# Performance work log

Measured on AMD Instinct MI355X. Metric: run time of the kernel, lower is better.

## Reference

```python
import jax, jax.numpy as jnp
import numpy as np


def _gcn_conv(x, src, dst, num_nodes, W, b):
    # GCNConv (PyG defaults): h = D^{-1/2} (A + I) D^{-1/2} (x @ W) + b
    h = x @ W  # [N, F_out]
    ones = jnp.ones(src.shape[0], dtype=h.dtype)
    deg = jax.ops.segment_sum(ones, dst, num_segments=num_nodes)  # in-degree incl. self loop
    dinv = jnp.where(deg > 0, jax.lax.rsqrt(deg), 0.0)
    norm = dinv[src] * dinv[dst]  # [E+N]
    msg = h[src] * norm[:, None]  # gather + scale (memory-bound)
    out = jax.ops.segment_sum(msg, dst, num_segments=num_nodes)
    return out + b


def setup_inputs() -> dict:
    key = jax.random.key(0)
    k1, k2, k3, k4 = jax.random.split(key, 4)
    N, E, D_IN, D_H, D_OUT = 100000, 1600000, 128, 64, 32
    x = jax.random.normal(k1, (N, D_IN), dtype=jnp.float32)
    edge_index = jax.random.randint(k2, (2, E), 0, N, dtype=jnp.int64)
    # Glorot-style init for weights, zero bias (as PyG reset_parameters)
    W1 = jax.random.normal(k3, (D_IN, D_H), dtype=jnp.float32) * (2.0 / (D_IN + D_H)) ** 0.5
    b1 = jnp.zeros((D_H,), dtype=jnp.float32)
    W2 = jax.random.normal(k4, (D_H, D_OUT), dtype=jnp.float32) * (2.0 / (D_H + D_OUT)) ** 0.5
    b2 = jnp.zeros((D_OUT,), dtype=jnp.float32)
    return {"x": x, "edge_index": edge_index, "W1": W1, "b1": b1, "W2": W2, "b2": b2}


def reference(x, edge_index, W1, b1, W2, b2):
    num_nodes = x.shape[0]
    # add self loops once (GCNConv default add_self_loops=True)
    loop = jnp.arange(num_nodes, dtype=edge_index.dtype)
    src = jnp.concatenate([edge_index[0], loop])
    dst = jnp.concatenate([edge_index[1], loop])
    h = jax.nn.relu(_gcn_conv(x, src, dst, num_nodes, W1, b1))
    # F.dropout(training=self.training): eval mode -> identity
    out = _gcn_conv(h, src, dst, num_nodes, W2, b2)
    return out
```

## Files before the change

### kernel.cpp

```cpp
#include <hip/hip_runtime.h>
#include <math.h>


#define THREADS 256
#define HTHREADS 512
#define PBLK 256
#define BSHIFT 8
#define AGG_NODES 64
#define CSR_LDS 2048

typedef _Float16 h8v __attribute__((ext_vector_type(8)));
typedef _Float16 h4v __attribute__((ext_vector_type(4)));

__device__ __forceinline__ int nt_ld_i(const int* p) {
    return __builtin_nontemporal_load(p);
}

__device__ __forceinline__ int detect64_block(const int* __restrict__ idx, int E,
                                              int* s_flag) {
    if (threadIdx.x == 0) *s_flag = 1;
    __syncthreads();
    int n = (E < 1024) ? E : 1024;
    for (int i = threadIdx.x; i < n; i += blockDim.x)
        if (idx[2 * i + 1] != 0) *s_flag = 0;
    __syncthreads();
    return *s_flag;
}

__global__ __launch_bounds__(HTHREADS) void k_hist(const int* __restrict__ idx, int E,
                                                   int* __restrict__ bh, int NB) {
    extern __shared__ int lh[];
    int is64 = detect64_block(idx, E, &lh[NB]);
    for (int t = threadIdx.x; t < NB; t += HTHREADS) lh[t] = 0;
    __syncthreads();
    int chunk = (E + PBLK - 1) / PBLK;
    int start = blockIdx.x * chunk;
    int end = min(start + chunk, E);
    for (int e = start + threadIdx.x; e < end; e += HTHREADS) {
        int d = is64 ? idx[2 * E + 2 * e] : idx[E + e];
        atomicAdd(&lh[d >> BSHIFT], 1);
    }
    __syncthreads();
    for (int t = threadIdx.x; t < NB; t += HTHREADS)
        bh[blockIdx.x * NB + t] = lh[t];
}

__global__ __launch_bounds__(THREADS) void k_colsum(const int* __restrict__ bh,
                                                    int* __restrict__ bcnt, int NB) {
    __shared__ int ws[4];
    int b = blockIdx.x;
    int v = bh[threadIdx.x * NB + b];
    int lane = threadIdx.x & 63, w = threadIdx.x >> 6;
#pragma unroll
    for (int o = 32; o; o >>= 1) v += __shfl_down(v, o);
    if (lane == 0) ws[w] = v;
    __syncthreads();
    if (threadIdx.x == 0) bcnt[b] = ws[0] + ws[1] + ws[2] + ws[3];
}

__global__ __launch_bounds__(THREADS) void k_scan(const int* __restrict__ cnt,
                                                  int* __restrict__ off, int NB) {
    __shared__ int wsum[4];
    __shared__ int carry_s;
    if (threadIdx.x == 0) carry_s = 0;
    __syncthreads();
    int t = threadIdx.x, lane = t & 63, w = t >> 6;
    for (int base = 0; base < NB; base += THREADS) {
        int i = base + t;
        int raw = (i < NB) ? cnt[i] : 0;
        int v = raw;
#pragma unroll
        for (int o = 1; o < 64; o <<= 1) {
            int u = __shfl_up(v, o);
            if (lane >= o) v += u;
        }
        if (lane == 63) wsum[w] = v;
        __syncthreads();
        int c0 = carry_s;
        int wadd = 0;
#pragma unroll
        for (int k = 0; k < 4; ++k) if (k < w) wadd += wsum[k];
        if (i < NB) off[i] = v - raw + wadd + c0;
        __syncthreads();
        if (t == 0) carry_s += wsum[0] + wsum[1] + wsum[2] + wsum[3];
        __syncthreads();
    }
    if (t == 0) off[NB] = carry_s;
}

__global__ __launch_bounds__(64) void k_bbase(const int* __restrict__ bh,
                                              const int* __restrict__ boff,
                                              int* __restrict__ bbase, int NB) {
    int b = blockIdx.x;
    int lane = threadIdx.x;
    int carry = boff[b];
    for (int base = 0; base < PBLK; base += 64) {
        int idx = (base + lane) * NB + b;
        int raw = bh[idx];
        int v = raw;
#pragma unroll
        for (int o = 1; o < 64; o <<= 1) {
            int u = __shfl_up(v, o);
            if (lane >= o) v += u;
        }
        bbase[idx] = carry + v - raw;
        carry += __shfl(v, 63);
    }
}

__global__ __launch_bounds__(HTHREADS) void k_partition(const int* __restrict__ idx, int E,
                                                        const int* __restrict__ bbase,
                                                        unsigned* __restrict__ pairs, int NB) {
    extern __shared__ int sm[];
    int* lbase = sm;
    int* lcur  = sm + NB;
    int is64 = detect64_block(idx, E, &lcur[NB]);
    for (int t = threadIdx.x; t < NB; t += HTHREADS) {
        lbase[t] = bbase[blockIdx.x * NB + t];
        lcur[t] = 0;
    }
    __syncthreads();
    int chunk = (E + PBLK - 1) / PBLK;
    int start = blockIdx.x * chunk;
    int end = min(start + chunk, E);
    for (int e = start + threadIdx.x; e < end; e += HTHREADS) {
        int s = is64 ? idx[2 * e] : idx[e];
        int d = is64 ? idx[2 * E + 2 * e] : idx[E + e];
        int b = d >> BSHIFT;
        int r = atomicAdd(&lcur[b], 1);
        pairs[lbase[b] + r] = (unsigned)s | ((unsigned)(d & 255) << 24);
    }
}

__global__ __launch_bounds__(THREADS) void k_sort(const unsigned* __restrict__ pairs,
                                                  const int* __restrict__ boff,
                                                  int* __restrict__ csr_src,
                                                  int* __restrict__ row_ptr,
                                                  float* __restrict__ dinv, int N, int NB) {
    __shared__ int cnt[256];
    __shared__ int cur[256];
    __shared__ int wsum[4];
    const int b = blockIdx.x, t = threadIdx.x;
    const int start = boff[b], end = boff[b + 1];
    cnt[t] = 0;
    __syncthreads();
    for (int j = start + t; j < end; j += THREADS)
        atomicAdd(&cnt[pairs[j] >> 24], 1);
    __syncthreads();
    int deg = cnt[t];
    int lane = t & 63, w = t >> 6;
    int v = deg;
#pragma unroll
    for (int o = 1; o < 64; o <<= 1) {
        int u = __shfl_up(v, o);
        if (lane >= o) v += u;
    }
    if (lane == 63) wsum[w] = v;
    __syncthreads();
    int wadd = 0;
#pragma unroll
    for (int k = 0; k < 4; ++k) if (k < w) wadd += wsum[k];
    int pos = start + (v - deg) + wadd;
    cur[t] = pos;
    int node = (b << BSHIFT) + t;
    if (node < N) {
        row_ptr[node] = pos;
        dinv[node] = rsqrtf((float)(deg + 1));
    }
    if (b == NB - 1 && t == 0) row_ptr[N] = end;
    __syncthreads();
    for (int j = start + t; j < end; j += THREADS) {
        unsigned p = pairs[j];
        int r = atomicAdd(&cur[p >> 24], 1);
        csr_src[r] = (int)(p & 0xFFFFFFu);
    }
}

__global__ __launch_bounds__(THREADS) void k_gemm1(const float* __restrict__ x,
                                                   const float* __restrict__ W,
                                                   const float* __restrict__ dinv,
                                                   _Float16* __restrict__ h, int N) {
    __shared__ float xs[64][68];
    __shared__ float ws[64][64];
    const int tid = threadIdx.x;
    const int brow = blockIdx.x * 64;
    const int lane = tid & 63, wv = tid >> 6;
    const int jc = (lane & 15) << 2;
    const int rb = (lane >> 4) + (wv << 2);
    float4 acc[4];
    acc[0] = acc[1] = acc[2] = acc[3] = make_float4(0.f, 0.f, 0.f, 0.f);

    for (int kt = 0; kt < 128; kt += 64) {
        for (int f = tid; f < 64 * 16; f += THREADS) {
            int r = f >> 4, k4 = (f & 15) << 2;
            int row = brow + r;
            float4 v = make_float4(0.f, 0.f, 0.f, 0.f);
            if (row < N) v = *(const float4*)&x[(size_t)row * 128 + kt + k4];
            *(float4*)&xs[r][k4] = v;
        }
        for (int f = tid; f < 64 * 16; f += THREADS) {
            int k = f >> 4, c4 = (f & 15) << 2;
            *(float4*)&ws[k][c4] = *(const float4*)&W[(size_t)(kt + k) * 64 + c4];
        }
        __syncthreads();
#pragma unroll
        for (int k = 0; k < 64; k += 4) {
            float4 a[4], b[4];
#pragma unroll
            for (int i = 0; i < 4; ++i) a[i] = *(const float4*)&xs[rb + (i << 4)][k];
#pragma unroll
            for (int kk = 0; kk < 4; ++kk) b[kk] = *(const float4*)&ws[k + kk][jc];
#pragma unroll
            for (int i = 0; i < 4; ++i) {
                const float* ai = (const float*)&a[i];
#pragma unroll
                for (int kk = 0; kk < 4; ++kk) {
                    float av = ai[kk];
                    acc[i].x += av * b[kk].x;
                    acc[i].y += av * b[kk].y;
                    acc[i].z += av * b[kk].z;
                    acc[i].w += av * b[kk].w;
                }
            }
        }
        __syncthreads();
    }
#pragma unroll
    for (int i = 0; i < 4; ++i) {
        int row = brow + rb + (i << 4);
        if (row < N) {
            float dn = dinv[row];
            h4v hv;
            hv.x = (_Float16)(acc[i].x * dn);
            hv.y = (_Float16)(acc[i].y * dn);
            hv.z = (_Float16)(acc[i].z * dn);
            hv.w = (_Float16)(acc[i].w * dn);
            *(h4v*)&h[(size_t)row * 64 + jc] = hv;
        }
    }
}

__global__ __launch_bounds__(THREADS) void k_agg1f(const int* __restrict__ row_ptr,
                                                   const int* __restrict__ csr,
                                                   const float* __restrict__ dinv,
                                                   const _Float16* __restrict__ hs,
                                                   const float* __restrict__ b1,
                                                   const float* __restrict__ W2,
                                                   _Float16* __restrict__ h2s, int N) {
    __shared__ float w2s[64][32];
    __shared__ float rowbuf[4][8][68];
    __shared__ int rp_s[AGG_NODES + 1];
    __shared__ float dinv_s[AGG_NODES];
    __shared__ int csr_s[CSR_LDS];
    const int tid = threadIdx.x;
    for (int f = tid; f < 64 * 8; f += THREADS) {
        int k = f >> 3, c4 = (f & 7) << 2;
        *(float4*)&w2s[k][c4] = *(const float4*)&W2[(size_t)k * 32 + c4];
    }
    const int nbase = blockIdx.x * AGG_NODES;
    const int nend = min(nbase + AGG_NODES, N);
    const int ncnt = nend - nbase;
    if (tid <= ncnt) rp_s[tid] = row_ptr[nbase + tid];
    if (tid < ncnt) dinv_s[tid] = dinv[nbase + tid];
    __syncthreads();
    const int seg0 = rp_s[0];
    const int seglen = rp_s[ncnt] - seg0;
    const bool inlds = (seglen <= CSR_LDS);
    if (inlds)
        for (int t = tid; t < seglen; t += THREADS) csr_s[t] = nt_ld_i(&csr[seg0 + t]);
    __syncthreads();

    const int wv = tid >> 6, lane = tid & 63;
    const int g = lane >> 3, fl = lane & 7;
    const int fb = fl << 3;

    for (int c = 0; c < 2; ++c) {
        const int nloc = (wv << 4) + (c << 3) + g;
        const bool act = (nloc < ncnt);
        const int node = nbase + nloc;
        const int start = act ? rp_s[nloc] : 0;
        const int end = act ? rp_s[nloc + 1] : 0;
        h8v acc0 = {0, 0, 0, 0, 0, 0, 0, 0};
        h8v acc1 = {0, 0, 0, 0, 0, 0, 0, 0};
        if (act) acc0 = *(const h8v*)&hs[(size_t)node * 64 + fb];
        if (inlds) {
            int j = start - seg0;
            const int e_ = end - seg0;
            for (; j + 1 < e_; j += 2) {
                int s0 = csr_s[j], s1 = csr_s[j + 1];
                acc0 += *(const h8v*)&hs[(size_t)s0 * 64 + fb];
                acc1 += *(const h8v*)&hs[(size_t)s1 * 64 + fb];
            }
            if (j < e_) acc0 += *(const h8v*)&hs[(size_t)csr_s[j] * 64 + fb];
        } else {
            int j = start;
            for (; j + 1 < end; j += 2) {
                int s0 = nt_ld_i(&csr[j]), s1 = nt_ld_i(&csr[j + 1]);
                acc0 += *(const h8v*)&hs[(size_t)s0 * 64 + fb];
                acc1 += *(const h8v*)&hs[(size_t)s1 * 64 + fb];
            }
            if (j < end) acc0 += *(const h8v*)&hs[(size_t)nt_ld_i(&csr[j]) * 64 + fb];
        }
        if (act) {
            const float dn = dinv_s[nloc];
            float4 bb0 = *(const float4*)&b1[fb];
            float4 bb1 = *(const float4*)&b1[fb + 4];
            float4 r0, r1;
            r0.x = fmaxf(dn * ((float)acc0[0] + (float)acc1[0]) + bb0.x, 0.f);
            r0.y = fmaxf(dn * ((float)acc0[1] + (float)acc1[1]) + bb0.y, 0.f);
            r0.z = fmaxf(dn * ((float)acc0[2] + (float)acc1[2]) + bb0.z, 0.f);
            r0.w = fmaxf(dn * ((float)acc0[3] + (float)acc1[3]) + bb0.w, 0.f);
            r1.x = fmaxf(dn * ((float)acc0[4] + (float)acc1[4]) + bb1.x, 0.f);
            r1.y = fmaxf(dn * ((float)acc0[5] + (float)acc1[5]) + bb1.y, 0.f);
            r1.z = fmaxf(dn * ((float)acc0[6] + (float)acc1[6]) + bb1.z, 0.f);
            r1.w = fmaxf(dn * ((float)acc0[7] + (float)acc1[7]) + bb1.w, 0.f);
            *(float4*)&rowbuf[wv][g][fb] = r0;
            *(float4*)&rowbuf[wv][g][fb + 4] = r1;
        }
        if (act) {
            float a0 = 0.f, a1 = 0.f, a2 = 0.f, a3 = 0.f;
            const int cb = fl << 2;
#pragma unroll
            for (int k = 0; k < 64; ++k) {
                float r = rowbuf[wv][g][k];
                a0 += r * w2s[k][cb + 0];
                a1 += r * w2s[k][cb + 1];
                a2 += r * w2s[k][cb + 2];
                a3 += r * w2s[k][cb + 3];
            }
            const float dn = dinv_s[nloc];
            h4v hv;
            hv.x = (_Float16)(dn * a0);
            hv.y = (_Float16)(dn * a1);
            hv.z = (_Float16)(dn * a2);
            hv.w = (_Float16)(dn * a3);
            *(h4v*)&h2s[(size_t)node * 32 + cb] = hv;
        }
    }
}

__global__ __launch_bounds__(THREADS) void k_agg2(const int* __restrict__ row_ptr,
                                                  const int* __restrict__ csr,
                                                  const float* __restrict__ dinv,
                                                  const _Float16* __restrict__ hs,
                                                  const float* __restrict__ b2,
                                                  float* __restrict__ out, int N) {
    __shared__ int rp_s[AGG_NODES + 1];
    __shared__ float dinv_s[AGG_NODES];
    __shared__ int csr_s[CSR_LDS];
    const int tid = threadIdx.x;
    const int nbase = blockIdx.x * AGG_NODES;
    const int nend = min(nbase + AGG_NODES, N);
    const int ncnt = nend - nbase;
    if (tid <= ncnt) rp_s[tid] = row_ptr[nbase + tid];
    if (tid < ncnt) dinv_s[tid] = dinv[nbase + tid];
    __syncthreads();
    const int seg0 = rp_s[0];
    const int seglen = rp_s[ncnt] - seg0;
    const bool inlds = (seglen <= CSR_LDS);
    if (inlds)
        for (int t = tid; t < seglen; t += THREADS) csr_s[t] = nt_ld_i(&csr[seg0 + t]);
    __syncthreads();

    const int wv = tid >> 6, lane = tid & 63;
    const int g = lane >> 2, fl = lane & 3;
    const int fb = fl << 3;

    const int nloc = (wv << 4) + g;
    const bool act = (nloc < ncnt);
    const int node = nbase + nloc;
    const int start = act ? rp_s[nloc] : 0;
    const int end = act ? rp_s[nloc + 1] : 0;
    h8v acc0 = {0, 0, 0, 0, 0, 0, 0, 0};
    h8v acc1 = {0, 0, 0, 0, 0, 0, 0, 0};
    if (act) acc0 = *(const h8v*)&hs[(size_t)node * 32 + fb];
    if (inlds) {
        int j = start - seg0;
        const int e_ = end - seg0;
        for (; j + 1 < e_; j += 2) {
            int s0 = csr_s[j], s1 = csr_s[j + 1];
            acc0 += *(const h8v*)&hs[(size_t)s0 * 32 + fb];
            acc1 += *(const h8v*)&hs[(size_t)s1 * 32 + fb];
        }
        if (j < e_) acc0 += *(const h8v*)&hs[(size_t)csr_s[j] * 32 + fb];
    } else {
        int j = start;
        for (; j + 1 < end; j += 2) {
            int s0 = nt_ld_i(&csr[j]), s1 = nt_ld_i(&csr[j + 1]);
            acc0 += *(const h8v*)&hs[(size_t)s0 * 32 + fb];
            acc1 += *(const h8v*)&hs[(size_t)s1 * 32 + fb];
        }
        if (j < end) acc0 += *(const h8v*)&hs[(size_t)nt_ld_i(&csr[j]) * 32 + fb];
    }
    if (act) {
        const float dn = dinv_s[nloc];
        float4 bb0 = *(const float4*)&b2[fb];
        float4 bb1 = *(const float4*)&b2[fb + 4];
        float4 r0, r1;
        r0.x = dn * ((float)acc0[0] + (float)acc1[0]) + bb0.x;
        r0.y = dn * ((float)acc0[1] + (float)acc1[1]) + bb0.y;
        r0.z = dn * ((float)acc0[2] + (float)acc1[2]) + bb0.z;
        r0.w = dn * ((float)acc0[3] + (float)acc1[3]) + bb0.w;
        r1.x = dn * ((float)acc0[4] + (float)acc1[4]) + bb1.x;
        r1.y = dn * ((float)acc0[5] + (float)acc1[5]) + bb1.y;
        r1.z = dn * ((float)acc0[6] + (float)acc1[6]) + bb1.z;
        r1.w = dn * ((float)acc0[7] + (float)acc1[7]) + bb1.w;
        *(float4*)&out[(size_t)node * 32 + fb] = r0;
        *(float4*)&out[(size_t)node * 32 + fb + 4] = r1;
    }
}

extern "C" void kernel_launch(void* const* d_in, const int* in_sizes, int n_in,
                              void* d_out, int out_size, void* d_ws, size_t ws_size,
                              hipStream_t stream) {
    const int N = in_sizes[0] / 128;
    const int E = in_sizes[1] / 2;
    const float* x  = (const float*)d_in[0];
    const int*   ei = (const int*)d_in[1];
    const float* W1 = (const float*)d_in[2];
    const float* b1 = (const float*)d_in[3];
    const float* W2 = (const float*)d_in[4];
    const float* b2 = (const float*)d_in[5];
    float* out = (float*)d_out;

    const int NB = (N + 255) >> BSHIFT;

    float*     dinv    = (float*)d_ws;
    _Float16*  h1b     = (_Float16*)(dinv + N);
    _Float16*  h2b     = h1b + (size_t)N * 64;
    int*       csr_src = (int*)(h2b + (size_t)N * 32);
    int*       row_ptr = csr_src + E;
    int*       bh      = row_ptr + N + 1;
    int*       bbase   = bh + (size_t)PBLK * NB;
    int*       bcnt    = bbase + (size_t)PBLK * NB;
    int*       boff    = bcnt + NB;
    unsigned*  pairs   = (unsigned*)h1b;

    k_hist<<<PBLK, HTHREADS, (NB + 1) * 4, stream>>>(ei, E, bh, NB);
    k_colsum<<<NB, THREADS, 0, stream>>>(bh, bcnt, NB);
    k_scan<<<1, THREADS, 0, stream>>>(bcnt, boff, NB);
    k_bbase<<<NB, 64, 0, stream>>>(bh, boff, bbase, NB);
    k_partition<<<PBLK, HTHREADS, (2 * NB + 1) * 4, stream>>>(ei, E, bbase, pairs, NB);
    k_sort<<<NB, THREADS, 0, stream>>>(pairs, boff, csr_src, row_ptr, dinv, N, NB);

    k_gemm1<<<(N + 63) / 64, THREADS, 0, stream>>>(x, W1, dinv, h1b, N);
    const int ablk = (N + AGG_NODES - 1) / AGG_NODES;
    k_agg1f<<<ablk, THREADS, 0, stream>>>(row_ptr, csr_src, dinv, h1b, b1, W2, h2b, N);
    k_agg2<<<ablk, THREADS, 0, stream>>>(row_ptr, csr_src, dinv, h2b, b2, out, N);
}
```

Before: 141.0 us.

## Use fp16 MFMA for first-layer GEMM with transposed weight tile

Replaces the scalar FP32 register-tiled GEMM in k_gemm1 with the 16x16x32 fp16 MFMA intrinsic. Both x and W are converted to half precision in LDS, with W stored transposed. This cuts ALU work for the x@W1 product, which is small compared with the whole pipeline. In exchange the output stores become scalar half writes, the weight transpose writes hit LDS with strided stores, and the inputs lose precision to fp16.

```diff
diff --git a/kernel.cpp b/kernel.cpp
--- a/kernel.cpp
+++ b/kernel.cpp
@@ -11,6 +11,7 @@
 
 typedef _Float16 h8v __attribute__((ext_vector_type(8)));
 typedef _Float16 h4v __attribute__((ext_vector_type(4)));
+typedef float f32x4 __attribute__((ext_vector_type(4)));
 
 __device__ __forceinline__ int nt_ld_i(const int* p) {
     return __builtin_nontemporal_load(p);
@@ -180,62 +181,51 @@
                                                    const float* __restrict__ W,
                                                    const float* __restrict__ dinv,
                                                    _Float16* __restrict__ h, int N) {
-    __shared__ float xs[64][68];
-    __shared__ float ws[64][64];
+    __shared__ _Float16 xs[64][136];
+    __shared__ _Float16 wsT[64][136];
     const int tid = threadIdx.x;
     const int brow = blockIdx.x * 64;
-    const int lane = tid & 63, wv = tid >> 6;
-    const int jc = (lane & 15) << 2;
-    const int rb = (lane >> 4) + (wv << 2);
-    float4 acc[4];
-    acc[0] = acc[1] = acc[2] = acc[3] = make_float4(0.f, 0.f, 0.f, 0.f);
-
-    for (int kt = 0; kt < 128; kt += 64) {
-        for (int f = tid; f < 64 * 16; f += THREADS) {
-            int r = f >> 4, k4 = (f & 15) << 2;
-            int row = brow + r;
-            float4 v = make_float4(0.f, 0.f, 0.f, 0.f);
-            if (row < N) v = *(const float4*)&x[(size_t)row * 128 + kt + k4];
-            *(float4*)&xs[r][k4] = v;
-        }
-        for (int f = tid; f < 64 * 16; f += THREADS) {
-            int k = f >> 4, c4 = (f & 15) << 2;
-            *(float4*)&ws[k][c4] = *(const float4*)&W[(size_t)(kt + k) * 64 + c4];
-        }
-        __syncthreads();
-#pragma unroll
-        for (int k = 0; k < 64; k += 4) {
-            float4 a[4], b[4];
-#pragma unroll
-            for (int i = 0; i < 4; ++i) a[i] = *(const float4*)&xs[rb + (i << 4)][k];
-#pragma unroll
-            for (int kk = 0; kk < 4; ++kk) b[kk] = *(const float4*)&ws[k + kk][jc];
-#pragma unroll
-            for (int i = 0; i < 4; ++i) {
-                const float* ai = (const float*)&a[i];
-#pragma unroll
-                for (int kk = 0; kk < 4; ++kk) {
-                    float av = ai[kk];
-                    acc[i].x += av * b[kk].x;
-                    acc[i].y += av * b[kk].y;
-                    acc[i].z += av * b[kk].z;
-                    acc[i].w += av * b[kk].w;
-                }
-            }
-        }
-        __syncthreads();
+    for (int f = tid; f < 64 * 32; f += THREADS) {
+        int r = f >> 5, c4 = (f & 31) << 2;
+        int row = brow + r;
+        float4 v = make_float4(0.f, 0.f, 0.f, 0.f);
+        if (row < N) v = *(const float4*)&x[(size_t)row * 128 + c4];
+        h4v hv;
+        hv.x = (_Float16)v.x; hv.y = (_Float16)v.y;
+        hv.z = (_Float16)v.z; hv.w = (_Float16)v.w;
+        *(h4v*)&xs[r][c4] = hv;
+    }
+    for (int f = tid; f < 128 * 16; f += THREADS) {
+        int k = f >> 4, n4 = (f & 15) << 2;
+        float4 w = *(const float4*)&W[(size_t)k * 64 + n4];
+        wsT[n4 + 0][k] = (_Float16)w.x;
+        wsT[n4 + 1][k] = (_Float16)w.y;
+        wsT[n4 + 2][k] = (_Float16)w.z;
+        wsT[n4 + 3][k] = (_Float16)w.w;
+    }
+    __syncthreads();
+    const int wv = tid >> 6, lane = tid & 63;
+    const int fr = lane & 15;
+    const int kg = lane >> 4;
+    f32x4 acc[4];
+    acc[0] = acc[1] = acc[2] = acc[3] = (f32x4){0.f, 0.f, 0.f, 0.f};
+#pragma unroll
+    for (int ks = 0; ks < 4; ++ks) {
+        h8v a = *(const h8v*)&xs[(wv << 4) + fr][(kg << 3) + (ks << 5)];
+#pragma unroll
+        for (int c = 0; c < 4; ++c) {
+            h8v b = *(const h8v*)&wsT[(c << 4) + fr][(kg << 3) + (ks << 5)];
+            acc[c] = __builtin_amdgcn_mfma_f32_16x16x32_f16(a, b, acc[c], 0, 0, 0);
+        }
     }
 #pragma unroll
     for (int i = 0; i < 4; ++i) {
-        int row = brow + rb + (i << 4);
+        int row = brow + (wv << 4) + (kg << 2) + i;
         if (row < N) {
             float dn = dinv[row];
-            h4v hv;
-            hv.x = (_Float16)(acc[i].x * dn);
-            hv.y = (_Float16)(acc[i].y * dn);
-            hv.z = (_Float16)(acc[i].z * dn);
-            hv.w = (_Float16)(acc[i].w * dn);
-            *(h4v*)&h[(size_t)row * 64 + jc] = hv;
+#pragma unroll
+            for (int c = 0; c < 4; ++c)
+                h[(size_t)row * 64 + (c << 4) + fr] = (_Float16)(acc[c][i] * dn);
         }
     }
 }
```

Measured after the change: 128.1 us. 9.2% less time.
